# Optimization experiments

Hardware: AMD Instinct MI355X
Metric: run time of the kernel (lower is better)

The kernel has to match this reference:

```python
import jax, jax.numpy as jnp
import numpy as np

NUM_HEADS = 16
HEAD_DIM = 128
VALUE_HEAD_DIM = 128
CHUNK = 1024
ROPE_BASE = 10000.0


def _rope(q, k, start):
    # q, k: (B, T, H, D). Rotate pairs (first half, second half) per RotaryEmbedding.
    B, T, H, D = q.shape
    half = D // 2
    inv_freq = jnp.exp(jnp.arange(half, dtype=jnp.float32) * (-np.log(ROPE_BASE) / half))
    pos = jnp.arange(T, dtype=jnp.float32) + jnp.float32(start)
    ang = pos[:, None] * inv_freq[None, :]            # (T, half)
    cos = jnp.cos(ang)[None, :, None, :].astype(q.dtype)
    sin = jnp.sin(ang)[None, :, None, :].astype(q.dtype)

    def rot(x):
        a, b = jnp.split(x, 2, axis=-1)
        return jnp.concatenate([a * cos - b * sin, b * cos + a * sin], axis=-1)

    return rot(q), rot(k)


def setup_inputs() -> dict:
    key = jax.random.key(0)
    k1, k2, k3 = jax.random.split(key, 3)
    B, L = 4, 4096
    q = jax.random.normal(k1, (B, L, NUM_HEADS, HEAD_DIM), dtype=jnp.float32)
    k = jax.random.normal(k2, (B, L, NUM_HEADS, HEAD_DIM), dtype=jnp.float32)
    v = jax.random.normal(k3, (B, L, NUM_HEADS, VALUE_HEAD_DIM), dtype=jnp.float32)
    return {"q": q, "k": k, "v": v, "start_index": 0}


def reference(q, k, v, start_index):
    # ChunkedSelfAttention.forward with cache=None, attn_mask=None, training=False:
    # RoPE at absolute positions, then causal SDPA within each chunk of size CHUNK.
    B, L, H, Dh = q.shape
    Dv = v.shape[-1]
    q, k = _rope(q, k, start_index)
    nc = L // CHUNK
    qc = q.reshape(B, nc, CHUNK, H, Dh)
    kc = k.reshape(B, nc, CHUNK, H, Dh)
    vc = v.reshape(B, nc, CHUNK, H, Dv)
    scale = 1.0 / np.sqrt(Dh).astype(np.float32)
    scores = jnp.einsum('bnqhd,bnkhd->bnhqk', qc, kc) * scale  # (B, nc, H, C, C)
    i = jnp.arange(CHUNK)
    causal = i[:, None] >= i[None, :]                          # (C, C)
    neg = jnp.asarray(jnp.finfo(scores.dtype).min, scores.dtype)
    scores = jnp.where(causal[None, None, None], scores, neg)
    attn = jax.nn.softmax(scores, axis=-1)
    out = jnp.einsum('bnhqk,bnkhd->bnqhd', attn, vc)
    return out.reshape(B, L, H, Dv)
```

## Files before the change

kernel.cpp:

```cpp
#include <hip/hip_runtime.h>


typedef __attribute__((ext_vector_type(2)))  float     f32x2;
typedef __attribute__((ext_vector_type(4)))  float     f32x4;
typedef __attribute__((ext_vector_type(16))) float     f32x16;
typedef __attribute__((ext_vector_type(8)))  _Float16  f16x8;
typedef unsigned int   u32;
typedef unsigned short u16;
typedef __attribute__((ext_vector_type(4))) unsigned int u32x4;

#define MFMA(a, b, c) __builtin_amdgcn_mfma_f32_32x32x16_f16(a, b, c, 0, 0, 0)

constexpr int Ll = 4096;
constexpr float QSCALE = 0.08838834764831845f * 1.4426950408889634f;

__device__ __forceinline__ f32x4 ld_f32x4(const void* p) { f32x4 v; __builtin_memcpy(&v, p, 16); return v; }
__device__ __forceinline__ f32x2 ld_f32x2(const void* p) { f32x2 v; __builtin_memcpy(&v, p, 8);  return v; }
__device__ __forceinline__ u32x4 ld_u32x4(const void* p) { u32x4 v; __builtin_memcpy(&v, p, 16); return v; }
__device__ __forceinline__ void  st_u32x4(void* p, u32x4 v) { __builtin_memcpy(p, &v, 16); }
__device__ __forceinline__ f16x8 ld_f16x8(const void* p) { f16x8 v; __builtin_memcpy(&v, p, 16); return v; }
__device__ __forceinline__ f16x8 ld_frag(const u32* dwp) {
  f16x8 v;
  __builtin_memcpy(&v, dwp, 8);
  __builtin_memcpy(((char*)&v) + 8, dwp + 2, 8);
  return v;
}
__device__ __forceinline__ u32 packh(_Float16 a, _Float16 b) {
  return (u32)__builtin_bit_cast(u16, a) | ((u32)__builtin_bit_cast(u16, b) << 16);
}

__global__ void rope_table_k(const int* __restrict__ startp, float* __restrict__ tab) {
  int idx = blockIdx.x * 256 + threadIdx.x;
  int t = idx >> 6, hid = idx & 63;
  float a = (float)hid * (-0.14391156831212878f);
  float invf = expf(a);
  float ang = (float)(t + startp[0]) * invf;
  tab[2 * idx]     = cosf(ang);
  tab[2 * idx + 1] = sinf(ang);
}

__global__ __launch_bounds__(256)
void prep_k_kernel(const float* __restrict__ Kg, const float* __restrict__ tab,
                   u32* __restrict__ Kh) {
  const int R    = blockIdx.x * 4 + (threadIdx.x >> 6);
  const int lane = threadIdx.x & 63;
  const int h  = R & 15;
  const int bt = R >> 4;
  const int b  = bt >> 12;
  const int t  = bt & 4095;
  const int c  = t >> 10;
  const int j  = (t >> 6) & 15;
  const int row = t & 63;
  const int GID = (b * 4 + c) * 16 + h;
  const int sw  = (row & 7) << 4;
  const int dc  = ((4 * lane) ^ sw) >> 1;
  f32x2 a = ld_f32x2(Kg + (size_t)R * 128 + dc);
  float p0 = __shfl_xor(a.x, 32);
  float p1 = __shfl_xor(a.y, 32);
  f32x4 cs = ld_f32x4(tab + (size_t)t * 128 + 2 * (dc & 63));
  const float sgn = (dc < 64) ? -1.0f : 1.0f;
  float o0 = a.x * cs.x + sgn * (p0 * cs.y);
  float o1 = a.y * cs.z + sgn * (p1 * cs.w);
  Kh[((size_t)(GID * 16 + j) * 64 + row) * 64 + lane] = packh((_Float16)o0, (_Float16)o1);
}

__global__ __launch_bounds__(256)
void prep_vt_kernel(const float* __restrict__ Vg, u32* __restrict__ VT) {
  __shared__ __align__(16) u32 tile[4096];
  const int gj  = blockIdx.x;
  const int GID = gj >> 4, j = gj & 15;
  const int h = GID & 15, c = (GID >> 4) & 3, b = GID >> 6;
  const int tid = threadIdx.x;
  const size_t rowbase = ((size_t)(b * 4096 + c * 1024 + j * 64)) * 16 + h;
  const int k  = tid >> 2;
  const int dq = tid & 3;
  u16* t16 = (u16*)tile;
  #pragma unroll
  for (int it = 0; it < 8; ++it) {
    int dv0 = dq * 4 + 16 * it;
    f32x4 v4 = ld_f32x4(Vg + (rowbase + (size_t)k * 16) * 128 + dv0);
    #pragma unroll
    for (int u = 0; u < 4; ++u) {
      int dv = dv0 + u;
      int ci = k ^ ((dv & 7) << 3);
      t16[dv * 64 + ci] = __builtin_bit_cast(u16, (_Float16)v4[u]);
    }
  }
  __syncthreads();
  const u32* tsrc = tile + 16 * tid;
  u32* dst = VT + (size_t)gj * 4096 + 16 * tid;
  #pragma unroll
  for (int u = 0; u < 4; ++u) st_u32x4(dst + 4 * u, ld_u32x4(tsrc + 4 * u));
}

#define ATT_STG 8192

__global__ __launch_bounds__(512, 2)
void attn_f16_k(const float* __restrict__ Qg, const u32* __restrict__ Kh,
                const u32* __restrict__ VT, float* __restrict__ Og,
                const float* __restrict__ tab) {
  __shared__ __align__(16) u32 lds[2 * ATT_STG];

  const int bx  = blockIdx.x;
  const int h   = bx & 15;
  const int p   = (bx >> 4) & 1;
  const int c   = (bx >> 5) & 3;
  const int b   = bx >> 7;
  const int tid = threadIdx.x;
  const int w   = tid >> 6;
  const int lane= tid & 63;
  const int l31 = lane & 31;
  const int lg2 = lane >> 5;

  const size_t cbase = (size_t)(b * Ll + c * 1024);
  const size_t hoff  = (size_t)h * 128;
  const int tb  = c * 1024;
  const int GID = (b * 4 + c) * 16 + h;
  const u32* khg = Kh + (size_t)GID * 16 * 4096;
  const u32* vtg = VT + (size_t)GID * 16 * 4096;

  u32x4 stg[4];
  auto issue = [&](int j) {
    #pragma unroll
    for (int i = 0; i < 4; ++i) {
      int ch = w + 8 * i;
      const u32* src = (ch < 16) ? (khg + (size_t)j * 4096 + ch * 256 + 4 * lane)
                                 : (vtg + (size_t)j * 4096 + (ch - 16) * 256 + 4 * lane);
      stg[i] = ld_u32x4(src);
    }
  };
  auto store_stage = [&](int s) {
    u32* dst0 = lds + (size_t)s * ATT_STG;
    #pragma unroll
    for (int i = 0; i < 4; ++i) {
      int ch = w + 8 * i;
      st_u32x4(dst0 + ch * 256 + 4 * lane, stg[i]);
    }
  };

  #pragma unroll 1
  for (int sp = 0; sp < 2; ++sp) {
    const int qs = sp ? p : (3 - p);
    const int qrow = qs * 256 + w * 32 + l31;

    const float* qbase = Qg + (cbase + qrow) * 2048 + hoff;
    float xq[8][8];
    #pragma unroll
    for (int ds = 0; ds < 8; ++ds) {
      const float* ptr = qbase + ds * 16 + lg2 * 8;
      f32x4 v0 = ld_f32x4(ptr);
      f32x4 v1 = ld_f32x4(ptr + 4);
      xq[ds][0]=v0.x; xq[ds][1]=v0.y; xq[ds][2]=v0.z; xq[ds][3]=v0.w;
      xq[ds][4]=v1.x; xq[ds][5]=v1.y; xq[ds][6]=v1.z; xq[ds][7]=v1.w;
    }
    const float* trowq = tab + (size_t)(tb + qrow) * 128 + lg2 * 16;
    #pragma unroll
    for (int ds = 0; ds < 4; ++ds) {
      #pragma unroll
      for (int i2 = 0; i2 < 4; ++i2) {
        f32x4 cs = ld_f32x4(trowq + ds * 32 + i2 * 4);
        int i0 = 2 * i2;
        float a0 = xq[ds][i0],     b0 = xq[ds + 4][i0];
        xq[ds][i0]     = a0 * cs.x - b0 * cs.y;
        xq[ds + 4][i0] = b0 * cs.x + a0 * cs.y;
        float a1 = xq[ds][i0 + 1], b1 = xq[ds + 4][i0 + 1];
        xq[ds][i0 + 1]     = a1 * cs.z - b1 * cs.w;
        xq[ds + 4][i0 + 1] = b1 * cs.z + a1 * cs.w;
      }
    }
    f16x8 qh[8];
    #pragma unroll
    for (int ds = 0; ds < 8; ++ds)
      #pragma unroll
      for (int i = 0; i < 8; ++i)
        qh[ds][i] = (_Float16)(xq[ds][i] * QSCALE);

    f32x16 O[4];
    #pragma unroll
    for (int n = 0; n < 4; ++n) O[n] = (f32x16)0.0f;
    float m2 = -1e30f, lsum = 0.0f;
    const int  nt    = 4 * (qs + 1);
    const int  jmaxw = 4 * qs + (w >> 1);
    const bool oddw  = w & 1;

    issue(0);
    store_stage(0);
    __syncthreads();

    for (int j = 0; j < nt; ++j) {
      const int s = j & 1;
      const bool more = (j + 1 < nt);
      if (more) issue(j + 1);

      if (j <= jmaxw) {
        const bool full = oddw || (j < jmaxw);
        const u32* KB = lds + (size_t)s * ATT_STG;
        const u32* VB = KB + 4096;
        const u32* kr0 = KB + (size_t)l31 * 64;
        const u32* kr1 = kr0 + 32 * 64;
        const int  swk = (l31 & 7) << 2;

        f32x16 S0 = (f32x16)0.0f, S1 = (f32x16)0.0f;
        __builtin_amdgcn_s_setprio(1);
        #pragma unroll
        for (int ds = 0; ds < 8; ++ds) {
          int dc = (8 * ds + 4 * lg2) ^ swk;
          S0 = MFMA(ld_f16x8(kr0 + dc), qh[ds], S0);
          if (full) S1 = MFMA(ld_f16x8(kr1 + dc), qh[ds], S1);
        }
        __builtin_amdgcn_s_setprio(0);

        if (j == jmaxw) {
          #pragma unroll
          for (int r = 0; r < 16; ++r) {
            int crow = (r & 3) + 8 * (r >> 2) + 4 * lg2;
            if (crow > l31) { if (oddw) S1[r] = -1e30f; else S0[r] = -1e30f; }
          }
        }

        float tm = S0[0];
        #pragma unroll
        for (int r = 1; r < 16; ++r) tm = fmaxf(tm, S0[r]);
        if (full) {
          #pragma unroll
          for (int r = 0; r < 16; ++r) tm = fmaxf(tm, S1[r]);
        }
        tm = fmaxf(tm, __shfl_xor(tm, 32));
        if (!__all(tm <= m2 + 8.0f)) {
          float m2n = fmaxf(m2, tm);
          float fac = exp2f(m2 - m2n);
          lsum *= fac;
          #pragma unroll
          for (int r = 0; r < 16; ++r) {
            int rq = (r & 3) + 8 * (r >> 2) + 4 * lg2;
            float fr = __shfl(fac, rq);
            O[0][r] *= fr; O[1][r] *= fr; O[2][r] *= fr; O[3][r] *= fr;
          }
          m2 = m2n;
        }
        u32 U[16];
        float ps = 0.0f;
        #pragma unroll
        for (int t = 0; t < 8; ++t) {
          float e0 = exp2f(S0[2 * t]     - m2);
          float e1 = exp2f(S0[2 * t + 1] - m2);
          U[t] = packh((_Float16)e0, (_Float16)e1);
          ps += e0 + e1;
        }
        if (full) {
          #pragma unroll
          for (int t = 0; t < 8; ++t) {
            float e0 = exp2f(S1[2 * t]     - m2);
            float e1 = exp2f(S1[2 * t + 1] - m2);
            U[8 + t] = packh((_Float16)e0, (_Float16)e1);
            ps += e0 + e1;
          }
        }
        ps += __shfl_xor(ps, 32);
        lsum += ps;

        __builtin_amdgcn_s_setprio(1);
        #pragma unroll
        for (int ks = 0; ks < 4; ++ks) {
          if (ks >= 2 && !full) continue;
          u32 a0 = U[4 * ks + 0], a1 = U[4 * ks + 1];
          u32 b0 = U[4 * ks + 2], b1 = U[4 * ks + 3];
          asm("v_permlane32_swap_b32 %0, %1" : "+v"(a0), "+v"(b0));
          asm("v_permlane32_swap_b32 %0, %1" : "+v"(a1), "+v"(b1));
          u32x4 t4; t4.x = a0; t4.y = a1; t4.z = b0; t4.w = b1;
          f16x8 pa = __builtin_bit_cast(f16x8, t4);
          int dcv = (8 * ks + 4 * lg2) ^ swk;
          #pragma unroll
          for (int n = 0; n < 4; ++n) {
            O[n] = MFMA(pa, ld_f16x8(VB + (size_t)(32 * n + l31) * 32 + dcv), O[n]);
          }
        }
        __builtin_amdgcn_s_setprio(0);
      }

      if (more) store_stage(s ^ 1);
      __syncthreads();
    }

    float inv = 1.0f / lsum;
    #pragma unroll
    for (int r = 0; r < 16; ++r) {
      int rq = (r & 3) + 8 * (r >> 2) + 4 * lg2;
      float fi = __shfl(inv, rq);
      float* orow = Og + (cbase + qs * 256 + w * 32 + rq) * 2048 + hoff + l31;
      orow[0]  = O[0][r] * fi;
      orow[32] = O[1][r] * fi;
      orow[64] = O[2][r] * fi;
      orow[96] = O[3][r] * fi;
    }
  }
}

#define KSTR 66
#define VSTR 34
#define KBUF (64 * KSTR)
#define VBUF (128 * VSTR)
#define STG  (KBUF + VBUF)

__global__ __launch_bounds__(512, 2)
void chunked_attn_fb(const float* __restrict__ Qg, const float* __restrict__ Kg,
                     const float* __restrict__ Vg, float* __restrict__ Og,
                     const float* __restrict__ tab) {
  __shared__ __align__(16) u32 lds[2 * STG];

  const int bx  = blockIdx.x;
  const int h   = bx & 15;
  const int p   = (bx >> 4) & 1;
  const int c   = (bx >> 5) & 3;
  const int b   = bx >> 7;
  const int tid = threadIdx.x;
  const int w   = tid >> 6;
  const int lane= tid & 63;
  const int l31 = lane & 31;
  const int lg2 = lane >> 5;

  const size_t cbase = (size_t)(b * Ll + c * 1024);
  const size_t hoff  = (size_t)h * 128;
  const int tb = c * 1024;

  f32x2 pk[8], pva[4], pvb[4];

  auto issue = [&](int j) {
    const float* kb_ = Kg + (cbase + (size_t)j * 64) * 2048 + hoff;
    const float* vb_ = Vg + (cbase + (size_t)j * 64) * 2048 + hoff;
    #pragma unroll
    for (int r = 0; r < 8; ++r)
      pk[r] = ld_f32x2(kb_ + (size_t)(8 * w + r) * 2048 + 2 * lane);
    #pragma unroll
    for (int rp = 0; rp < 4; ++rp) {
      const float* vr = vb_ + (size_t)(8 * w + 2 * rp) * 2048 + 2 * lane;
      pva[rp] = ld_f32x2(vr);
      pvb[rp] = ld_f32x2(vr + 2048);
    }
  };

  auto xform = [&](int j, int s) {
    u32* KB = lds + s * STG;
    u32* VB = KB + KBUF;
    const float* tbase = tab + (size_t)(tb + j * 64) * 128 + 4 * l31;
    f32x4 cs[8];
    #pragma unroll
    for (int r = 0; r < 8; ++r)
      cs[r] = ld_f32x4(tbase + (size_t)(8 * w + r) * 128);
    const float sgn = (lane < 32) ? -1.0f : 1.0f;
    #pragma unroll
    for (int r = 0; r < 8; ++r) {
      float a0 = pk[r].x, a1 = pk[r].y;
      float p0 = __shfl_xor(a0, 32), p1 = __shfl_xor(a1, 32);
      float o0 = a0 * cs[r].x + sgn * (p0 * cs[r].y);
      float o1 = a1 * cs[r].z + sgn * (p1 * cs[r].w);
      KB[(8 * w + r) * KSTR + lane] = packh((_Float16)o0, (_Float16)o1);
    }
    #pragma unroll
    for (int rp = 0; rp < 4; ++rp) {
      int kp = 4 * w + rp;
      VB[(2 * lane) * VSTR + kp]     = packh((_Float16)pva[rp].x, (_Float16)pvb[rp].x);
      VB[(2 * lane + 1) * VSTR + kp] = packh((_Float16)pva[rp].y, (_Float16)pvb[rp].y);
    }
  };

  #pragma unroll 1
  for (int sp = 0; sp < 2; ++sp) {
    const int qs = sp ? p : (3 - p);
    const int qrow = qs * 256 + w * 32 + l31;

    const float* qbase = Qg + (cbase + qrow) * 2048 + hoff;
    float xq[8][8];
    #pragma unroll
    for (int ds = 0; ds < 8; ++ds) {
      const float* ptr = qbase + ds * 16 + lg2 * 8;
      f32x4 v0 = ld_f32x4(ptr);
      f32x4 v1 = ld_f32x4(ptr + 4);
      xq[ds][0]=v0.x; xq[ds][1]=v0.y; xq[ds][2]=v0.z; xq[ds][3]=v0.w;
      xq[ds][4]=v1.x; xq[ds][5]=v1.y; xq[ds][6]=v1.z; xq[ds][7]=v1.w;
    }
    const float* trowq = tab + (size_t)(tb + qrow) * 128 + lg2 * 16;
    #pragma unroll
    for (int ds = 0; ds < 4; ++ds) {
      #pragma unroll
      for (int i2 = 0; i2 < 4; ++i2) {
        f32x4 cs = ld_f32x4(trowq + ds * 32 + i2 * 4);
        int i0 = 2 * i2;
        float a0 = xq[ds][i0],     b0 = xq[ds + 4][i0];
        xq[ds][i0]     = a0 * cs.x - b0 * cs.y;
        xq[ds + 4][i0] = b0 * cs.x + a0 * cs.y;
        float a1 = xq[ds][i0 + 1], b1 = xq[ds + 4][i0 + 1];
        xq[ds][i0 + 1]     = a1 * cs.z - b1 * cs.w;
        xq[ds + 4][i0 + 1] = b1 * cs.z + a1 * cs.w;
      }
    }
    f16x8 qh[8];
    #pragma unroll
    for (int ds = 0; ds < 8; ++ds)
      #pragma unroll
      for (int i = 0; i < 8; ++i)
        qh[ds][i] = (_Float16)(xq[ds][i] * QSCALE);

    f32x16 O[4];
    #pragma unroll
    for (int n = 0; n < 4; ++n) O[n] = (f32x16)0.0f;
    float m2 = -1e30f, lsum = 0.0f;
    const int  nt    = 4 * (qs + 1);
    const int  jmaxw = 4 * qs + (w >> 1);
    const bool oddw  = w & 1;

    issue(0);
    xform(0, 0);
    __syncthreads();

    for (int j = 0; j < nt; ++j) {
      const int s = j & 1;
      const bool more = (j + 1 < nt);
      if (more) issue(j + 1);

      if (j <= jmaxw) {
        const bool full = oddw || (j < jmaxw);
        const u32* KB = lds + s * STG;
        const u32* VB = KB + KBUF;
        const u32* kr0 = KB + (size_t)l31 * KSTR + lg2 * 4;
        const u32* kr1 = kr0 + (size_t)32 * KSTR;

        f32x16 S0 = (f32x16)0.0f, S1 = (f32x16)0.0f;
        __builtin_amdgcn_s_setprio(1);
        #pragma unroll
        for (int ds = 0; ds < 8; ++ds) {
          S0 = MFMA(ld_frag(kr0 + ds * 8), qh[ds], S0);
          if (full) S1 = MFMA(ld_frag(kr1 + ds * 8), qh[ds], S1);
        }
        __builtin_amdgcn_s_setprio(0);

        if (j == jmaxw) {
          #pragma unroll
          for (int r = 0; r < 16; ++r) {
            int crow = (r & 3) + 8 * (r >> 2) + 4 * lg2;
            if (crow > l31) { if (oddw) S1[r] = -1e30f; else S0[r] = -1e30f; }
          }
        }

        float tm = S0[0];
        #pragma unroll
        for (int r = 1; r < 16; ++r) tm = fmaxf(tm, S0[r]);
        if (full) {
          #pragma unroll
          for (int r = 0; r < 16; ++r) tm = fmaxf(tm, S1[r]);
        }
        tm = fmaxf(tm, __shfl_xor(tm, 32));
        if (!__all(tm <= m2 + 8.0f)) {
          float m2n = fmaxf(m2, tm);
          float fac = exp2f(m2 - m2n);
          lsum *= fac;
          #pragma unroll
          for (int r = 0; r < 16; ++r) {
            int rq = (r & 3) + 8 * (r >> 2) + 4 * lg2;
            float fr = __shfl(fac, rq);
            O[0][r] *= fr; O[1][r] *= fr; O[2][r] *= fr; O[3][r] *= fr;
          }
          m2 = m2n;
        }
        u32 U[16];
        float ps = 0.0f;
        #pragma unroll
        for (int t = 0; t < 8; ++t) {
          float e0 = exp2f(S0[2 * t]     - m2);
          float e1 = exp2f(S0[2 * t + 1] - m2);
          U[t] = packh((_Float16)e0, (_Float16)e1);
          ps += e0 + e1;
        }
        if (full) {
          #pragma unroll
          for (int t = 0; t < 8; ++t) {
            float e0 = exp2f(S1[2 * t]     - m2);
            float e1 = exp2f(S1[2 * t + 1] - m2);
            U[8 + t] = packh((_Float16)e0, (_Float16)e1);
            ps += e0 + e1;
          }
        }
        ps += __shfl_xor(ps, 32);
        lsum += ps;

        __builtin_amdgcn_s_setprio(1);
        #pragma unroll
        for (int ks = 0; ks < 4; ++ks) {
          if (ks >= 2 && !full) continue;
          u32 a0 = U[4 * ks + 0], a1 = U[4 * ks + 1];
          u32 b0 = U[4 * ks + 2], b1 = U[4 * ks + 3];
          asm("v_permlane32_swap_b32 %0, %1" : "+v"(a0), "+v"(b0));
          asm("v_permlane32_swap_b32 %0, %1" : "+v"(a1), "+v"(b1));
          u32x4 t4; t4.x = a0; t4.y = a1; t4.z = b0; t4.w = b1;
          f16x8 pa = __builtin_bit_cast(f16x8, t4);
          #pragma unroll
          for (int n = 0; n < 4; ++n) {
            const u32* vp = VB + (size_t)(32 * n + l31) * VSTR + 8 * ks + 4 * lg2;
            O[n] = MFMA(pa, ld_frag(vp), O[n]);
          }
        }
        __builtin_amdgcn_s_setprio(0);
      }

      if (more) xform(j + 1, s ^ 1);
      __syncthreads();
    }

    float inv = 1.0f / lsum;
    #pragma unroll
    for (int r = 0; r < 16; ++r) {
      int rq = (r & 3) + 8 * (r >> 2) + 4 * lg2;
      float fi = __shfl(inv, rq);
      float* orow = Og + (cbase + qs * 256 + w * 32 + rq) * 2048 + hoff + l31;
      orow[0]  = O[0][r] * fi;
      orow[32] = O[1][r] * fi;
      orow[64] = O[2][r] * fi;
      orow[96] = O[3][r] * fi;
    }
  }
}

extern "C" void kernel_launch(void* const* d_in, const int* in_sizes, int n_in,
                              void* d_out, int out_size, void* d_ws, size_t ws_size,
                              hipStream_t stream) {
  const float* q = (const float*)d_in[0];
  const float* k = (const float*)d_in[1];
  const float* v = (const float*)d_in[2];
  const int* start = (const int*)d_in[3];
  float* out = (float*)d_out;

  float* tab = (float*)d_ws;
  const size_t KH_OFFB = 2u * 1024 * 1024;
  const size_t VT_OFFB = KH_OFFB + 64u * 1024 * 1024;
  const size_t NEED = VT_OFFB + 64u * 1024 * 1024;

  rope_table_k<<<dim3(1024), dim3(256), 0, stream>>>(start, tab);

  if (ws_size >= NEED) {
    u32* Kh = (u32*)((char*)d_ws + KH_OFFB);
    u32* VT = (u32*)((char*)d_ws + VT_OFFB);
    prep_k_kernel<<<dim3(65536), dim3(256), 0, stream>>>(k, tab, Kh);
    prep_vt_kernel<<<dim3(4096), dim3(256), 0, stream>>>(v, VT);
    attn_f16_k<<<dim3(512), dim3(512), 0, stream>>>(q, Kh, VT, out, tab);
  } else {
    chunked_attn_fb<<<dim3(512), dim3(512), 0, stream>>>(q, k, v, out, tab);
  }
}
```

Before: 273.5 us.

## Give each wave two query tiles to reuse K/V LDS fragments across them

The attention kernel now runs 4 waves per block instead of 8. Each wave processes 64 query rows as two 32-row tiles, sharing every K and V fragment loaded from LDS between both tiles' MFMAs. Causal work per key tile is reassigned per wave, the staging loop now has each wave load 8 chunks, and the fp16 packing uses the cvt_pkrtz intrinsic. This halves LDS reads per MFMA but doubles accumulator and Q registers per wave and lowers the number of waves per CU, which may reduce latency hiding.

```diff
diff --git a/kernel.cpp b/kernel.cpp
--- a/kernel.cpp
+++ b/kernel.cpp
@@ -27,6 +27,10 @@
 }
 __device__ __forceinline__ u32 packh(_Float16 a, _Float16 b) {
   return (u32)__builtin_bit_cast(u16, a) | ((u32)__builtin_bit_cast(u16, b) << 16);
+}
+__device__ __forceinline__ u32 pkrtz(float a, float b) {
+  auto v = __builtin_amdgcn_cvt_pkrtz(a, b);
+  u32 r; __builtin_memcpy(&r, &v, 4); return r;
 }
 
 __global__ void rope_table_k(const int* __restrict__ startp, float* __restrict__ tab) {
@@ -93,13 +97,11 @@
   for (int u = 0; u < 4; ++u) st_u32x4(dst + 4 * u, ld_u32x4(tsrc + 4 * u));
 }
 
-#define ATT_STG 8192
-
-__global__ __launch_bounds__(512, 2)
+__global__ __launch_bounds__(256, 1)
 void attn_f16_k(const float* __restrict__ Qg, const u32* __restrict__ Kh,
                 const u32* __restrict__ VT, float* __restrict__ Og,
                 const float* __restrict__ tab) {
-  __shared__ __align__(16) u32 lds[2 * ATT_STG];
+  __shared__ __align__(16) u32 lds[2 * 8192];
 
   const int bx  = blockIdx.x;
   const int h   = bx & 15;
@@ -119,30 +121,24 @@
   const u32* khg = Kh + (size_t)GID * 16 * 4096;
   const u32* vtg = VT + (size_t)GID * 16 * 4096;
 
-  u32x4 stg[4];
+  u32x4 stg[8];
   auto issue = [&](int j) {
     #pragma unroll
-    for (int i = 0; i < 4; ++i) {
-      int ch = w + 8 * i;
+    for (int i = 0; i < 8; ++i) {
+      int ch = w * 8 + i;
       const u32* src = (ch < 16) ? (khg + (size_t)j * 4096 + ch * 256 + 4 * lane)
                                  : (vtg + (size_t)j * 4096 + (ch - 16) * 256 + 4 * lane);
       stg[i] = ld_u32x4(src);
     }
   };
   auto store_stage = [&](int s) {
-    u32* dst0 = lds + (size_t)s * ATT_STG;
-    #pragma unroll
-    for (int i = 0; i < 4; ++i) {
-      int ch = w + 8 * i;
-      st_u32x4(dst0 + ch * 256 + 4 * lane, stg[i]);
-    }
+    u32* dst0 = lds + (size_t)s * 8192;
+    #pragma unroll
+    for (int i = 0; i < 8; ++i)
+      st_u32x4(dst0 + (w * 8 + i) * 256 + 4 * lane, stg[i]);
   };
 
-  #pragma unroll 1
-  for (int sp = 0; sp < 2; ++sp) {
-    const int qs = sp ? p : (3 - p);
-    const int qrow = qs * 256 + w * 32 + l31;
-
+  auto loadq = [&](int qrow, f16x8* qh) {
     const float* qbase = Qg + (cbase + qrow) * 2048 + hoff;
     float xq[8][8];
     #pragma unroll
@@ -168,20 +164,28 @@
         xq[ds + 4][i0 + 1] = b1 * cs.z + a1 * cs.w;
       }
     }
-    f16x8 qh[8];
     #pragma unroll
     for (int ds = 0; ds < 8; ++ds)
       #pragma unroll
       for (int i = 0; i < 8; ++i)
         qh[ds][i] = (_Float16)(xq[ds][i] * QSCALE);
-
-    f32x16 O[4];
-    #pragma unroll
-    for (int n = 0; n < 4; ++n) O[n] = (f32x16)0.0f;
-    float m2 = -1e30f, lsum = 0.0f;
-    const int  nt    = 4 * (qs + 1);
-    const int  jmaxw = 4 * qs + (w >> 1);
-    const bool oddw  = w & 1;
+  };
+
+  #pragma unroll 1
+  for (int sp = 0; sp < 2; ++sp) {
+    const int qs = sp ? p : (3 - p);
+    const int qb = qs * 256 + w * 64;
+
+    f16x8 qhA[8], qhB[8];
+    loadq(qb + l31, qhA);
+    loadq(qb + 32 + l31, qhB);
+
+    f32x16 OA[4], OB[4];
+    #pragma unroll
+    for (int n = 0; n < 4; ++n) { OA[n] = (f32x16)0.0f; OB[n] = (f32x16)0.0f; }
+    float m2A = -1e30f, lsA = 0.0f, m2B = -1e30f, lsB = 0.0f;
+    const int j0 = 4 * qs + w;
+    const int nt = 4 * (qs + 1);
 
     issue(0);
     store_stage(0);
@@ -192,107 +196,130 @@
       const bool more = (j + 1 < nt);
       if (more) issue(j + 1);
 
-      if (j <= jmaxw) {
-        const bool full = oddw || (j < jmaxw);
-        const u32* KB = lds + (size_t)s * ATT_STG;
-        const u32* VB = KB + 4096;
+      if (j <= j0) {
+        const bool diag = (j == j0);
+        const u32* KB  = lds + (size_t)s * 8192;
+        const u32* VB  = KB + 4096;
         const u32* kr0 = KB + (size_t)l31 * 64;
-        const u32* kr1 = kr0 + 32 * 64;
+        const u32* kr1 = kr0 + 2048;
         const int  swk = (l31 & 7) << 2;
 
-        f32x16 S0 = (f32x16)0.0f, S1 = (f32x16)0.0f;
-        __builtin_amdgcn_s_setprio(1);
+        f32x16 S0A = (f32x16)0.0f, S1A = (f32x16)0.0f;
+        f32x16 S0B = (f32x16)0.0f, S1B = (f32x16)0.0f;
         #pragma unroll
         for (int ds = 0; ds < 8; ++ds) {
           int dc = (8 * ds + 4 * lg2) ^ swk;
-          S0 = MFMA(ld_f16x8(kr0 + dc), qh[ds], S0);
-          if (full) S1 = MFMA(ld_f16x8(kr1 + dc), qh[ds], S1);
-        }
-        __builtin_amdgcn_s_setprio(0);
-
-        if (j == jmaxw) {
+          f16x8 k0 = ld_f16x8(kr0 + dc);
+          f16x8 k1 = ld_f16x8(kr1 + dc);
+          S0A = MFMA(k0, qhA[ds], S0A);
+          S0B = MFMA(k0, qhB[ds], S0B);
+          if (!diag) S1A = MFMA(k1, qhA[ds], S1A);
+          S1B = MFMA(k1, qhB[ds], S1B);
+        }
+
+        if (diag) {
           #pragma unroll
           for (int r = 0; r < 16; ++r) {
             int crow = (r & 3) + 8 * (r >> 2) + 4 * lg2;
-            if (crow > l31) { if (oddw) S1[r] = -1e30f; else S0[r] = -1e30f; }
-          }
-        }
-
-        float tm = S0[0];
-        #pragma unroll
-        for (int r = 1; r < 16; ++r) tm = fmaxf(tm, S0[r]);
-        if (full) {
-          #pragma unroll
-          for (int r = 0; r < 16; ++r) tm = fmaxf(tm, S1[r]);
-        }
-        tm = fmaxf(tm, __shfl_xor(tm, 32));
-        if (!__all(tm <= m2 + 8.0f)) {
-          float m2n = fmaxf(m2, tm);
-          float fac = exp2f(m2 - m2n);
-          lsum *= fac;
-          #pragma unroll
-          for (int r = 0; r < 16; ++r) {
-            int rq = (r & 3) + 8 * (r >> 2) + 4 * lg2;
-            float fr = __shfl(fac, rq);
-            O[0][r] *= fr; O[1][r] *= fr; O[2][r] *= fr; O[3][r] *= fr;
-          }
-          m2 = m2n;
-        }
-        u32 U[16];
-        float ps = 0.0f;
-        #pragma unroll
-        for (int t = 0; t < 8; ++t) {
-          float e0 = exp2f(S0[2 * t]     - m2);
-          float e1 = exp2f(S0[2 * t + 1] - m2);
-          U[t] = packh((_Float16)e0, (_Float16)e1);
-          ps += e0 + e1;
-        }
-        if (full) {
+            if (crow > l31) { S0A[r] = -1e30f; S1B[r] = -1e30f; }
+          }
+        }
+
+        u32 UA[16], UB[16];
+        auto softmax = [&](f32x16& S0, f32x16& S1, bool full, float& m2,
+                           float& lsum, u32* U, f32x16* O) {
+          float tm = S0[0];
+          #pragma unroll
+          for (int r = 1; r < 16; ++r) tm = fmaxf(tm, S0[r]);
+          if (full) {
+            #pragma unroll
+            for (int r = 0; r < 16; ++r) tm = fmaxf(tm, S1[r]);
+          }
+          tm = fmaxf(tm, __shfl_xor(tm, 32));
+          if (!__all(tm <= m2 + 8.0f)) {
+            float m2n = fmaxf(m2, tm);
+            float fac = exp2f(m2 - m2n);
+            lsum *= fac;
+            #pragma unroll
+            for (int r = 0; r < 16; ++r) {
+              int rq = (r & 3) + 8 * (r >> 2) + 4 * lg2;
+              float fr = __shfl(fac, rq);
+              O[0][r] *= fr; O[1][r] *= fr; O[2][r] *= fr; O[3][r] *= fr;
+            }
+            m2 = m2n;
+          }
+          float ps = 0.0f;
           #pragma unroll
           for (int t = 0; t < 8; ++t) {
-            float e0 = exp2f(S1[2 * t]     - m2);
-            float e1 = exp2f(S1[2 * t + 1] - m2);
-            U[8 + t] = packh((_Float16)e0, (_Float16)e1);
+            float e0 = exp2f(S0[2 * t]     - m2);
+            float e1 = exp2f(S0[2 * t + 1] - m2);
+            U[t] = pkrtz(e0, e1);
             ps += e0 + e1;
           }
-        }
-        ps += __shfl_xor(ps, 32);
-        lsum += ps;
-
-        __builtin_amdgcn_s_setprio(1);
+          if (full) {
+            #pragma unroll
+            for (int t = 0; t < 8; ++t) {
+              float e0 = exp2f(S1[2 * t]     - m2);
+              float e1 = exp2f(S1[2 * t + 1] - m2);
+              U[8 + t] = pkrtz(e0, e1);
+              ps += e0 + e1;
+            }
+          }
+          ps += __shfl_xor(ps, 32);
+          lsum += ps;
+        };
+        softmax(S0A, S1A, !diag, m2A, lsA, UA, OA);
+        softmax(S0B, S1B, true,  m2B, lsB, UB, OB);
+
         #pragma unroll
         for (int ks = 0; ks < 4; ++ks) {
-          if (ks >= 2 && !full) continue;
-          u32 a0 = U[4 * ks + 0], a1 = U[4 * ks + 1];
-          u32 b0 = U[4 * ks + 2], b1 = U[4 * ks + 3];
-          asm("v_permlane32_swap_b32 %0, %1" : "+v"(a0), "+v"(b0));
-          asm("v_permlane32_swap_b32 %0, %1" : "+v"(a1), "+v"(b1));
-          u32x4 t4; t4.x = a0; t4.y = a1; t4.z = b0; t4.w = b1;
-          f16x8 pa = __builtin_bit_cast(f16x8, t4);
+          const bool aAct = !(diag && ks >= 2);
+          f16x8 paA, paB;
+          {
+            u32 a0 = UB[4 * ks + 0], a1 = UB[4 * ks + 1];
+            u32 b0 = UB[4 * ks + 2], b1 = UB[4 * ks + 3];
+            asm("v_permlane32_swap_b32 %0, %1" : "+v"(a0), "+v"(b0));
+            asm("v_permlane32_swap_b32 %0, %1" : "+v"(a1), "+v"(b1));
+            u32x4 t4; t4.x = a0; t4.y = a1; t4.z = b0; t4.w = b1;
+            paB = __builtin_bit_cast(f16x8, t4);
+          }
+          if (aAct) {
+            u32 a0 = UA[4 * ks + 0], a1 = UA[4 * ks + 1];
+            u32 b0 = UA[4 * ks + 2], b1 = UA[4 * ks + 3];
+            asm("v_permlane32_swap_b32 %0, %1" : "+v"(a0), "+v"(b0));
+            asm("v_permlane32_swap_b32 %0, %1" : "+v"(a1), "+v"(b1));
+            u32x4 t4; t4.x = a0; t4.y = a1; t4.z = b0; t4.w = b1;
+            paA = __builtin_bit_cast(f16x8, t4);
+          }
           int dcv = (8 * ks + 4 * lg2) ^ swk;
           #pragma unroll
           for (int n = 0; n < 4; ++n) {
-            O[n] = MFMA(pa, ld_f16x8(VB + (size_t)(32 * n + l31) * 32 + dcv), O[n]);
-          }
-        }
-        __builtin_amdgcn_s_setprio(0);
+            f16x8 vf = ld_f16x8(VB + (size_t)(32 * n + l31) * 32 + dcv);
+            if (aAct) OA[n] = MFMA(paA, vf, OA[n]);
+            OB[n] = MFMA(paB, vf, OB[n]);
+          }
+        }
       }
 
       if (more) store_stage(s ^ 1);
       __syncthreads();
     }
 
-    float inv = 1.0f / lsum;
-    #pragma unroll
-    for (int r = 0; r < 16; ++r) {
-      int rq = (r & 3) + 8 * (r >> 2) + 4 * lg2;
-      float fi = __shfl(inv, rq);
-      float* orow = Og + (cbase + qs * 256 + w * 32 + rq) * 2048 + hoff + l31;
-      orow[0]  = O[0][r] * fi;
-      orow[32] = O[1][r] * fi;
-      orow[64] = O[2][r] * fi;
-      orow[96] = O[3][r] * fi;
-    }
+    auto epi = [&](float lsum, f32x16* O, int qbg) {
+      float inv = 1.0f / lsum;
+      #pragma unroll
+      for (int r = 0; r < 16; ++r) {
+        int rq = (r & 3) + 8 * (r >> 2) + 4 * lg2;
+        float fi = __shfl(inv, rq);
+        float* orow = Og + (cbase + qbg + rq) * 2048 + hoff + l31;
+        orow[0]  = O[0][r] * fi;
+        orow[32] = O[1][r] * fi;
+        orow[64] = O[2][r] * fi;
+        orow[96] = O[3][r] * fi;
+      }
+    };
+    epi(lsA, OA, qb);
+    epi(lsB, OB, qb + 32);
   }
 }
 
@@ -541,7 +568,7 @@
     u32* VT = (u32*)((char*)d_ws + VT_OFFB);
     prep_k_kernel<<<dim3(65536), dim3(256), 0, stream>>>(k, tab, Kh);
     prep_vt_kernel<<<dim3(4096), dim3(256), 0, stream>>>(v, VT);
-    attn_f16_k<<<dim3(512), dim3(512), 0, stream>>>(q, Kh, VT, out, tab);
+    attn_f16_k<<<dim3(512), dim3(256), 0, stream>>>(q, Kh, VT, out, tab);
   } else {
     chunked_attn_fb<<<dim3(512), dim3(512), 0, stream>>>(q, k, v, out, tab);
   }
```

Measured after the change: 364.0 us. +33.1%, slower.

## Switch attention LDS staging to padded-stride layout with split fragment loads

Applied to the files above, without the earlier changes.

The K/V staging buffers in the main f16 attention kernel move from a dense 64-dword-per-row layout to padded strides (66 for K, 34 for V), matching the fallback kernel. Stores and fragment loads are split into two 8-byte accesses to fit the unaligned padded rows. The softmax row max now uses a tree reduction, and f16 packing uses the packed round-toward-zero convert. The padding is meant to reduce LDS bank conflicts, but the XOR swizzle is still applied and 16-byte accesses become pairs of 8-byte ones, which may add LDS instructions.

```diff
diff --git a/kernel.cpp b/kernel.cpp
--- a/kernel.cpp
+++ b/kernel.cpp
@@ -14,19 +14,31 @@
 constexpr int Ll = 4096;
 constexpr float QSCALE = 0.08838834764831845f * 1.4426950408889634f;
 
+#define KSTR 66
+#define VSTR 34
+#define KBUF (64 * KSTR)
+#define STG  (KBUF + 128 * VSTR)
+
 __device__ __forceinline__ f32x4 ld_f32x4(const void* p) { f32x4 v; __builtin_memcpy(&v, p, 16); return v; }
 __device__ __forceinline__ f32x2 ld_f32x2(const void* p) { f32x2 v; __builtin_memcpy(&v, p, 8);  return v; }
 __device__ __forceinline__ u32x4 ld_u32x4(const void* p) { u32x4 v; __builtin_memcpy(&v, p, 16); return v; }
 __device__ __forceinline__ void  st_u32x4(void* p, u32x4 v) { __builtin_memcpy(p, &v, 16); }
-__device__ __forceinline__ f16x8 ld_f16x8(const void* p) { f16x8 v; __builtin_memcpy(&v, p, 16); return v; }
 __device__ __forceinline__ f16x8 ld_frag(const u32* dwp) {
   f16x8 v;
   __builtin_memcpy(&v, dwp, 8);
   __builtin_memcpy(((char*)&v) + 8, dwp + 2, 8);
   return v;
 }
+__device__ __forceinline__ void st_frag(u32* dwp, u32x4 v) {
+  __builtin_memcpy(dwp, &v, 8);
+  __builtin_memcpy(dwp + 2, ((char*)&v) + 8, 8);
+}
 __device__ __forceinline__ u32 packh(_Float16 a, _Float16 b) {
   return (u32)__builtin_bit_cast(u16, a) | ((u32)__builtin_bit_cast(u16, b) << 16);
+}
+__device__ __forceinline__ u32 pkrtz(float a, float b) {
+  auto v = __builtin_amdgcn_cvt_pkrtz(a, b);
+  u32 r; __builtin_memcpy(&r, &v, 4); return r;
 }
 
 __global__ void rope_table_k(const int* __restrict__ startp, float* __restrict__ tab) {
@@ -93,13 +105,11 @@
   for (int u = 0; u < 4; ++u) st_u32x4(dst + 4 * u, ld_u32x4(tsrc + 4 * u));
 }
 
-#define ATT_STG 8192
-
 __global__ __launch_bounds__(512, 2)
 void attn_f16_k(const float* __restrict__ Qg, const u32* __restrict__ Kh,
                 const u32* __restrict__ VT, float* __restrict__ Og,
                 const float* __restrict__ tab) {
-  __shared__ __align__(16) u32 lds[2 * ATT_STG];
+  __shared__ __align__(16) u32 lds[2 * STG];
 
   const int bx  = blockIdx.x;
   const int h   = bx & 15;
@@ -130,12 +140,30 @@
     }
   };
   auto store_stage = [&](int s) {
-    u32* dst0 = lds + (size_t)s * ATT_STG;
+    u32* dst0 = lds + (size_t)s * STG;
     #pragma unroll
     for (int i = 0; i < 4; ++i) {
       int ch = w + 8 * i;
-      st_u32x4(dst0 + ch * 256 + 4 * lane, stg[i]);
-    }
+      u32* dst;
+      if (ch < 16) {
+        int row = 4 * ch + (lane >> 4);
+        dst = dst0 + row * KSTR + 4 * (lane & 15);
+      } else {
+        int row = 8 * (ch - 16) + (lane >> 3);
+        dst = dst0 + KBUF + row * VSTR + 4 * (lane & 7);
+      }
+      st_frag(dst, stg[i]);
+    }
+  };
+
+  auto vmax16 = [](const f32x16& S) {
+    float a0 = fmaxf(S[0], S[1]),   a1 = fmaxf(S[2], S[3]);
+    float a2 = fmaxf(S[4], S[5]),   a3 = fmaxf(S[6], S[7]);
+    float a4 = fmaxf(S[8], S[9]),   a5 = fmaxf(S[10], S[11]);
+    float a6 = fmaxf(S[12], S[13]), a7 = fmaxf(S[14], S[15]);
+    float b0 = fmaxf(a0, a1), b1 = fmaxf(a2, a3);
+    float b2 = fmaxf(a4, a5), b3 = fmaxf(a6, a7);
+    return fmaxf(fmaxf(b0, b1), fmaxf(b2, b3));
   };
 
   #pragma unroll 1
@@ -194,10 +222,10 @@
 
       if (j <= jmaxw) {
         const bool full = oddw || (j < jmaxw);
-        const u32* KB = lds + (size_t)s * ATT_STG;
-        const u32* VB = KB + 4096;
-        const u32* kr0 = KB + (size_t)l31 * 64;
-        const u32* kr1 = kr0 + 32 * 64;
+        const u32* KB = lds + (size_t)s * STG;
+        const u32* VB = KB + KBUF;
+        const u32* kr0 = KB + (size_t)l31 * KSTR;
+        const u32* kr1 = kr0 + 32 * KSTR;
         const int  swk = (l31 & 7) << 2;
 
         f32x16 S0 = (f32x16)0.0f, S1 = (f32x16)0.0f;
@@ -205,8 +233,8 @@
         #pragma unroll
         for (int ds = 0; ds < 8; ++ds) {
           int dc = (8 * ds + 4 * lg2) ^ swk;
-          S0 = MFMA(ld_f16x8(kr0 + dc), qh[ds], S0);
-          if (full) S1 = MFMA(ld_f16x8(kr1 + dc), qh[ds], S1);
+          S0 = MFMA(ld_frag(kr0 + dc), qh[ds], S0);
+          if (full) S1 = MFMA(ld_frag(kr1 + dc), qh[ds], S1);
         }
         __builtin_amdgcn_s_setprio(0);
 
@@ -218,13 +246,8 @@
           }
         }
 
-        float tm = S0[0];
-        #pragma unroll
-        for (int r = 1; r < 16; ++r) tm = fmaxf(tm, S0[r]);
-        if (full) {
-          #pragma unroll
-          for (int r = 0; r < 16; ++r) tm = fmaxf(tm, S1[r]);
-        }
+        float tm = vmax16(S0);
+        if (full) tm = fmaxf(tm, vmax16(S1));
         tm = fmaxf(tm, __shfl_xor(tm, 32));
         if (!__all(tm <= m2 + 8.0f)) {
           float m2n = fmaxf(m2, tm);
@@ -244,7 +267,7 @@
         for (int t = 0; t < 8; ++t) {
           float e0 = exp2f(S0[2 * t]     - m2);
           float e1 = exp2f(S0[2 * t + 1] - m2);
-          U[t] = packh((_Float16)e0, (_Float16)e1);
+          U[t] = pkrtz(e0, e1);
           ps += e0 + e1;
         }
         if (full) {
@@ -252,7 +275,7 @@
           for (int t = 0; t < 8; ++t) {
             float e0 = exp2f(S1[2 * t]     - m2);
             float e1 = exp2f(S1[2 * t + 1] - m2);
-            U[8 + t] = packh((_Float16)e0, (_Float16)e1);
+            U[8 + t] = pkrtz(e0, e1);
             ps += e0 + e1;
           }
         }
@@ -272,7 +295,7 @@
           int dcv = (8 * ks + 4 * lg2) ^ swk;
           #pragma unroll
           for (int n = 0; n < 4; ++n) {
-            O[n] = MFMA(pa, ld_f16x8(VB + (size_t)(32 * n + l31) * 32 + dcv), O[n]);
+            O[n] = MFMA(pa, ld_frag(VB + (size_t)(32 * n + l31) * VSTR + dcv), O[n]);
           }
         }
         __builtin_amdgcn_s_setprio(0);
@@ -295,12 +318,6 @@
     }
   }
 }
-
-#define KSTR 66
-#define VSTR 34
-#define KBUF (64 * KSTR)
-#define VBUF (128 * VSTR)
-#define STG  (KBUF + VBUF)
 
 __global__ __launch_bounds__(512, 2)
 void chunked_attn_fb(const float* __restrict__ Qg, const float* __restrict__ Kg,
```

Measured after the change: 287.0 us. +4.9%, slower.
